# Optimization experiments

Measured on AMD Instinct MI355X. Metric: run time of the kernel, lower is better.

The kernel has to match this reference:

```python
import jax, jax.numpy as jnp
import numpy as np

V, H, S, B, T = 32000, 1024, 512, 16, 128
SOS = 1  # config['special_tokens']['SOS'] assumed = 1


def setup_inputs() -> dict:
    key = jax.random.key(0)
    ks = jax.random.split(key, 16)
    s = 0.02
    return {
        "encoder_outputs": jax.random.normal(ks[0], (B, S, H), jnp.float32),
        "encoder_h": jax.random.normal(ks[1], (1, B, H), jnp.float32),
        "encoder_c": jax.random.normal(ks[2], (1, B, H), jnp.float32),
        "embedding": jax.random.normal(ks[3], (V, H), jnp.float32) * s,
        "Wq": jax.random.normal(ks[4], (H, H), jnp.float32) * s,
        "bq": jnp.zeros((H,), jnp.float32),
        "Wk": jax.random.normal(ks[5], (H, H), jnp.float32) * s,
        "bk": jnp.zeros((H,), jnp.float32),
        "Wv": jax.random.normal(ks[6], (H, H), jnp.float32) * s,
        "bv": jnp.zeros((H,), jnp.float32),
        "W_ih": jax.random.normal(ks[7], (4 * H, 2 * H), jnp.float32) * s,
        "b_ih": jnp.zeros((4 * H,), jnp.float32),
        "W_hh": jax.random.normal(ks[8], (4 * H, H), jnp.float32) * s,
        "b_hh": jnp.zeros((4 * H,), jnp.float32),
        "W_out": jax.random.normal(ks[9], (V, H), jnp.float32) * s,
        "b_out": jnp.zeros((V,), jnp.float32),
    }


def reference(encoder_outputs, encoder_h, encoder_c, embedding,
              Wq, bq, Wk, bk, Wv, bv,
              W_ih, b_ih, W_hh, b_hh, W_out, b_out):
    h0 = encoder_h[0]  # [B,H]
    c0 = encoder_c[0]
    # key/value projections of encoder outputs are constant across steps
    K = jnp.einsum('bsh,dh->bsd', encoder_outputs, Wk) + bk   # [B,S,H]
    Vl = jnp.einsum('bsh,dh->bsd', encoder_outputs, Wv) + bv  # [B,S,H]
    # decoder input is always SOS (source never updates it when target_tensor is None)
    emb = jnp.broadcast_to(embedding[SOS], (h0.shape[0], H))  # [B,H]
    scale = 1.0 / jnp.sqrt(jnp.float32(H))
    # 1x1 look-ahead mask (query seq_len == 1) is a no-op -> omitted

    def step(carry, _):
        h, c = carry
        q = h @ Wq.T + bq                                 # [B,H]
        scores = jnp.einsum('bh,bsh->bs', q, K) * scale   # [B,S]
        w = jax.nn.softmax(scores, axis=-1)
        ctx = jnp.einsum('bs,bsh->bh', w, Vl)             # [B,H]
        x = jnp.concatenate([emb, ctx], axis=-1)          # [B,2H] (embedded, attn)
        gates = x @ W_ih.T + b_ih + h @ W_hh.T + b_hh     # [B,4H]
        i, f, g, o = jnp.split(gates, 4, axis=-1)         # torch LSTM gate order i,f,g,o
        c2 = jax.nn.sigmoid(f) * c + jax.nn.sigmoid(i) * jnp.tanh(g)
        h2 = jax.nn.sigmoid(o) * jnp.tanh(c2)
        logits = h2 @ W_out.T + b_out                     # [B,V]
        return (h2, c2), logits

    (hT, cT), outs = jax.lax.scan(step, (h0, c0), None, length=T)  # outs [T,B,V]
    outs = jnp.transpose(outs, (1, 0, 2))                          # [B,T,V]
    log_probs = jax.nn.log_softmax(outs, axis=-1)
    return log_probs, (hT[None], cT[None])
```

## Files before the change

kernel.cpp:

```cpp
#include <hip/hip_runtime.h>
#include <hip/hip_bf16.h>
#include <math.h>

typedef short short8 __attribute__((ext_vector_type(8)));
typedef short short4v __attribute__((ext_vector_type(4)));
typedef float f32x4 __attribute__((ext_vector_type(4)));
typedef unsigned long long u64;

#define DEVI __device__ __forceinline__

DEVI float bf2f(short s){ union{unsigned u; float f;} x; x.u = ((unsigned)(unsigned short)s) << 16; return x.f; }

DEVI void st_u32v(unsigned* p, unsigned v){ __hip_atomic_store(p, v, __ATOMIC_RELAXED, __HIP_MEMORY_SCOPE_SYSTEM); }
DEVI unsigned ld_u32v(const unsigned* p){ return __hip_atomic_load(p, __ATOMIC_RELAXED, __HIP_MEMORY_SCOPE_SYSTEM); }
DEVI u64  ld_u64v(const u64* p){ return __hip_atomic_load(p, __ATOMIC_RELAXED, __HIP_MEMORY_SCOPE_SYSTEM); }
DEVI unsigned bfbits(float f){ __hip_bfloat16 h = __float2bfloat16(f); unsigned short b; __builtin_memcpy(&b,&h,2); return (unsigned)b; }

constexpr size_t o_wout   = 0;
constexpr size_t o_encbf  = 0;
constexpr size_t o_kbf    = 16777216;
constexpr size_t o_wkbf   = 33554432;
constexpr size_t o_wvbf   = 35651584;
constexpr size_t o_wqtbf  = 37748736;
constexpr size_t o_vt     = 41943040;
constexpr size_t o_kq     = 65536000;
constexpr size_t o_vbf    = o_kq    + 16777216;
constexpr size_t o_wih2   = o_vbf   + 16777216;
constexpr size_t o_whh    = o_wih2  + 8388608;
constexpr size_t o_hall   = o_whh   + 8388608;
constexpr size_t o_gconst = o_hall  + 4194304;
constexpr size_t o_sb     = o_gconst+ 16384;
constexpr size_t o_hv     = o_sb    + 32768;
constexpr size_t o_ev     = o_hv    + 65536;
constexpr size_t o_cv     = o_ev    + 32768;

__global__ void k_convert(const float* __restrict__ src, __hip_bfloat16* __restrict__ dst, int n){
  int i = (blockIdx.x*blockDim.x + threadIdx.x)*4;
  int stride = gridDim.x*blockDim.x*4;
  for (; i < n; i += stride){
    float4 v = *(const float4*)(src+i);
    __hip_bfloat16 o[4] = {__float2bfloat16(v.x),__float2bfloat16(v.y),__float2bfloat16(v.z),__float2bfloat16(v.w)};
    *(short4v*)(dst+i) = *(const short4v*)o;
  }
}

__global__ void k_tcvt(const float* __restrict__ src, __hip_bfloat16* __restrict__ dst){
  __shared__ float tile[64][65];
  int i0 = blockIdx.y*64, j0 = blockIdx.x*64;
  int tr = threadIdx.x >> 6, tc = threadIdx.x & 63;
  for (int p=0;p<16;p++){ int r = p*4 + tr; tile[r][tc] = src[(size_t)(i0+r)*1024 + j0+tc]; }
  __syncthreads();
  for (int p=0;p<16;p++){ int r = p*4 + tr; dst[(size_t)(j0+r)*1024 + i0+tc] = __float2bfloat16(tile[tc][r]); }
}

__global__ void k_extract(const float* __restrict__ src, __hip_bfloat16* __restrict__ dst){
  int i = blockIdx.x*blockDim.x + threadIdx.x;
  int stride = gridDim.x*blockDim.x;
  for (; i < 4096*1024; i += stride){
    int r = i >> 10, c = i & 1023;
    dst[i] = __float2bfloat16(src[((size_t)r << 11) + 1024 + c]);
  }
}

__global__ void k_init(const float* __restrict__ eh, unsigned* __restrict__ base){
  int i = blockIdx.x*blockDim.x + threadIdx.x;
  if (i < 16384) base[i] = bfbits(eh[i]);
  else if (i < 40960) base[i] = 0u;
}

__global__ void k_gconst(const float* __restrict__ emb, const float* __restrict__ Wih,
                         const float* __restrict__ bih, const float* __restrict__ bhh,
                         float* __restrict__ gc){
  int w = threadIdx.x >> 6, lane = threadIdx.x & 63;
  int n = blockIdx.x*4 + w;
  const float* er = emb + 1024;
  const float* wr = Wih + (size_t)n*2048;
  float acc = 0.f;
  for (int q=0;q<16;q++){ int k = lane*16+q; acc += er[k]*wr[k]; }
  for (int off=32; off; off>>=1) acc += __shfl_xor(acc, off);
  if (lane==0) gc[n] = acc + bih[n] + bhh[n];
}

__global__ void k_sb(const __hip_bfloat16* __restrict__ Kb, const float* __restrict__ bq,
                     float* __restrict__ sb){
  int w = threadIdx.x >> 6, lane = threadIdx.x & 63;
  int r = blockIdx.x*4 + w;
  const __hip_bfloat16* kr = Kb + (size_t)r*1024;
  float acc = 0.f;
  for (int q=0;q<16;q++){ int k = lane*16+q; acc += __bfloat162float(kr[k])*bq[k]; }
  for (int off=32; off; off>>=1) acc += __shfl_xor(acc, off);
  if (lane==0) sb[r] = acc * 0.03125f;
}

__global__ void k_vtrans(const __hip_bfloat16* __restrict__ V, __hip_bfloat16* __restrict__ VT){
  __shared__ short t[64][65];
  int b = blockIdx.z, s0 = blockIdx.y*64, h0 = blockIdx.x*64;
  int r = threadIdx.x >> 6, c = threadIdx.x & 63;
  const short* vp = (const short*)V + ((size_t)(b*512 + s0))*1024 + h0;
  #pragma unroll
  for (int p=0;p<16;p++) t[p*4+r][c] = vp[(size_t)(p*4+r)*1024 + c];
  __syncthreads();
  short* op = (short*)VT + ((size_t)(b*1024 + h0))*512 + s0;
  #pragma unroll
  for (int p=0;p<16;p++) op[(size_t)(p*4+r)*512 + c] = t[c][p*4+r];
}

template<int EPI>
__global__ __launch_bounds__(256) void k_gemm(const __hip_bfloat16* __restrict__ A,
    const __hip_bfloat16* __restrict__ Bm, const float* __restrict__ bias,
    void* __restrict__ Cp, int M, int N, int K, float scale){
  __shared__ __hip_bfloat16 sA[128*40];
  __shared__ __hip_bfloat16 sB[128*40];
  int tid = threadIdx.x;
  int lane = tid & 63, w = tid >> 6;
  int wr = w >> 1, wc = w & 1;
  int m0 = blockIdx.y*128, n0 = blockIdx.x*128;
  int lrow = lane & 15, lk = lane >> 4;
  f32x4 acc[4][4] = {};
  for (int k0 = 0; k0 < K; k0 += 32){
    __syncthreads();
    #pragma unroll
    for (int l0 = 0; l0 < 1024; l0 += 256){
      int l = l0 + tid;
      int half = l >> 9;
      int ch = l & 511;
      int row = ch >> 2, seg = ch & 3;
      const __hip_bfloat16* src = half ? (Bm + (size_t)(n0+row)*K + k0 + seg*8)
                                       : (A  + (size_t)(m0+row)*K + k0 + seg*8);
      __hip_bfloat16* dst = (half ? sB : sA) + row*40 + seg*8;
      *(short8*)dst = *(const short8*)src;
    }
    __syncthreads();
    short8 af[4], bfq[4];
    #pragma unroll
    for (int mi=0;mi<4;mi++) af[mi]  = *(short8*)(sA + (wr*64+mi*16+lrow)*40 + lk*8);
    #pragma unroll
    for (int ni=0;ni<4;ni++) bfq[ni] = *(short8*)(sB + (wc*64+ni*16+lrow)*40 + lk*8);
    #pragma unroll
    for (int mi=0;mi<4;mi++)
      #pragma unroll
      for (int ni=0;ni<4;ni++)
        acc[mi][ni] = __builtin_amdgcn_mfma_f32_16x16x32_bf16(af[mi], bfq[ni], acc[mi][ni], 0,0,0);
  }
  int crow0 = (lane>>4)*4;
  int ccol = lane & 15;
  #pragma unroll
  for (int mi=0;mi<4;mi++)
    #pragma unroll
    for (int ni=0;ni<4;ni++){
      int gn = n0 + wc*64 + ni*16 + ccol;
      float bv = bias ? bias[gn] : 0.0f;
      #pragma unroll
      for (int j=0;j<4;j++){
        int gm = m0 + wr*64 + mi*16 + crow0 + j;
        float v = acc[mi][ni][j]*scale + bv;
        if (EPI==0){
          ((__hip_bfloat16*)Cp)[(size_t)gm*N + gn] = __float2bfloat16(v);
        } else {
          int tt = gm >> 4, bb = gm & 15;
          ((float*)Cp)[(size_t)(bb*128+tt)*N + gn] = v;
        }
      }
    }
}

__global__ __launch_bounds__(256, 1) void k_decode(
    const __hip_bfloat16* __restrict__ KQ, const __hip_bfloat16* __restrict__ VT,
    const float* __restrict__ sb, const __hip_bfloat16* __restrict__ Whh,
    const __hip_bfloat16* __restrict__ Wih2, const float* __restrict__ gconst,
    const float* __restrict__ ec,
    unsigned* __restrict__ hv, unsigned* __restrict__ ev,
    unsigned* __restrict__ cv, __hip_bfloat16* __restrict__ hall,
    float* __restrict__ outH, float* __restrict__ outC)
{
  __shared__ __attribute__((aligned(16))) __hip_bfloat16 h4L[4][1032];
  __shared__ __attribute__((aligned(16))) float eL[528];
  __shared__ __attribute__((aligned(16))) float sPf[1024];
  __shared__ float sE[32];
  __shared__ __attribute__((aligned(16))) __hip_bfloat16 sCtx[64];
  __shared__ float sSb[32];
  __shared__ float sGc[64];
  __shared__ float sRed[4];

  const int tid = threadIdx.x;
  const int lane = tid & 63, wv = tid >> 6;
  const int l16 = lane & 15, lhi = lane >> 4;
  const int blk = blockIdx.x;
  const int xcd = blk & 7, slot = blk >> 3;
  const int grp = xcd >> 1, half = xcd & 1;
  const int bloc = half*2 + (slot >> 4);
  const int chunk = slot & 15;
  const int g4 = grp*4;
  const int b = g4 + bloc;
  const int j0 = (half*32 + slot) * 16;

  short8 wfrag[64];
  {
    const __hip_bfloat16* wsrc = (wv < 2) ? Whh : Wih2;
    const int koff = (wv & 1) * 512;
    #pragma unroll
    for (int tt = 0; tt < 4; tt++)
      #pragma unroll
      for (int kt = 0; kt < 16; kt++)
        wfrag[tt*16+kt] = *(const short8*)(wsrc + (size_t)(tt*1024 + j0 + l16)*1024 + koff + kt*32 + lhi*8);
  }
  if (tid < 32) sSb[tid] = sb[b*512 + chunk*32 + tid];
  if (tid < 64) sGc[(tid>>4)*16 + (tid&15)] = gconst[(tid>>4)*1024 + j0 + (tid&15)];
  float creg = 0.f;
  if (tid < 64) creg = ec[(size_t)(g4 + (tid>>4))*1024 + j0 + (tid&15)];

  const __hip_bfloat16* kqBlk = KQ + ((size_t)(b*512 + chunk*32))*1024;
  const int ar = (l16 < 4) ? l16 : 3;
  const short8 zfrag = {};
  f32x4 gacc[4] = {};

  const unsigned* snH = hv + (size_t)g4*1024 + lane*16;
  const unsigned* snE = ev + (size_t)b*512 + (lane & 15)*32;
  const unsigned* snC = cv + (size_t)(g4 + (lane>>4))*1024 + (lane&15)*64;

  for (int st = 0; st < 128; ++st){
    const unsigned wantH = (unsigned)st;
    const unsigned wantN = (unsigned)(st+1);

    { unsigned v; do { v = ld_u32v(snH); } while (!__all((int)((v>>16) == wantH))); }
    {
      const u64* s0 = (const u64*)(hv + (size_t)b*1024) + tid*2;
      u64 a0, a1; bool ok;
      do {
        a0 = ld_u64v(s0); a1 = ld_u64v(s0+1);
        ok = (((unsigned)a0>>16)==wantH) && ((unsigned)(a0>>48)==wantH)
          && (((unsigned)a1>>16)==wantH) && ((unsigned)(a1>>48)==wantH);
      } while(!ok);
      short4v o = { (short)(unsigned)a0, (short)(a0>>32), (short)(unsigned)a1, (short)(a1>>32) };
      *(short4v*)&h4L[bloc][tid*4] = o;
    }
    __syncthreads();
    {
      int row = tid >> 3, kx = tid & 7;
      const __hip_bfloat16* kp = kqBlk + (size_t)row*1024 + kx*8;
      float acc = 0.f;
      #pragma unroll
      for (int q = 0; q < 16; q++){
        short8 kv = *(const short8*)(kp + q*64);
        short8 hv8 = *(const short8*)&h4L[bloc][kx*8 + q*64];
        #pragma unroll
        for (int e2 = 0; e2 < 8; e2++) acc += bf2f(hv8[e2]) * bf2f(kv[e2]);
      }
      acc += __shfl_xor(acc, 1); acc += __shfl_xor(acc, 2); acc += __shfl_xor(acc, 4);
      if (kx == 0)
        st_u32v(&ev[(size_t)b*512 + chunk*32 + row], bfbits(expf(acc + sSb[row])) | (wantN<<16));
    }
    #pragma unroll
    for (int rr = 1; rr < 4; rr++){
      int r = (bloc + rr) & 3;
      const u64* s0 = (const u64*)(hv + (size_t)(g4 + r)*1024) + tid*2;
      u64 a0, a1; bool ok;
      do {
        a0 = ld_u64v(s0); a1 = ld_u64v(s0+1);
        ok = (((unsigned)a0>>16)==wantH) && ((unsigned)(a0>>48)==wantH)
          && (((unsigned)a1>>16)==wantH) && ((unsigned)(a1>>48)==wantH);
      } while(!ok);
      short4v o = { (short)(unsigned)a0, (short)(a0>>32), (short)(unsigned)a1, (short)(a1>>32) };
      *(short4v*)&h4L[r][tid*4] = o;
    }
    __syncthreads();
    if (wv < 2){
      const int ko = (wv & 1) * 512;
      #pragma unroll
      for (int kt = 0; kt < 16; kt++){
        short8 a = *(const short8*)&h4L[ar][ko + kt*32 + lhi*8];
        a = (l16 < 4) ? a : zfrag;
        #pragma unroll
        for (int tt = 0; tt < 4; tt++)
          gacc[tt] = __builtin_amdgcn_mfma_f32_16x16x32_bf16(a, wfrag[tt*16+kt], gacc[tt], 0,0,0);
      }
    }

    { unsigned v; do { v = ld_u32v(snE); } while (!__all((int)((v>>16) == wantN))); }
    {
      const u64* s = (const u64*)(ev + (size_t)b*512) + tid;
      u64 v;
      do { v = ld_u64v(s); }
      while(!((((unsigned)v>>16)==wantN) && ((unsigned)(v>>48)==wantN)));
      float e0 = bf2f((short)(unsigned)v), e1 = bf2f((short)(v>>32));
      int i0 = tid*2, pad = (tid>>6)<<2;
      eL[i0 + pad] = e0; eL[i0+1 + pad] = e1;
      float lp = e0 + e1;
      for (int off=32; off; off>>=1) lp += __shfl_xor(lp, off);
      if (lane == 0) sRed[wv] = lp;
    }
    __syncthreads();
    {
      float Linv = 1.0f/(sRed[0]+sRed[1]+sRed[2]+sRed[3]);
      int hloc = tid >> 2, sc = (tid & 3)*128;
      const __hip_bfloat16* vp = VT + ((size_t)(b*1024 + chunk*64 + hloc))*512 + sc;
      const float* epp = eL + sc + ((sc>>7)<<2);
      float a = 0.f;
      #pragma unroll
      for (int q = 0; q < 16; q++){
        short8 vv = *(const short8*)(vp + q*8);
        float4 e0 = *(const float4*)(epp + q*8);
        float4 e1 = *(const float4*)(epp + q*8 + 4);
        a += e0.x*bf2f(vv[0]) + e0.y*bf2f(vv[1]) + e0.z*bf2f(vv[2]) + e0.w*bf2f(vv[3]);
        a += e1.x*bf2f(vv[4]) + e1.y*bf2f(vv[5]) + e1.z*bf2f(vv[6]) + e1.w*bf2f(vv[7]);
      }
      a += __shfl_xor(a, 1); a += __shfl_xor(a, 2);
      if ((tid & 3) == 0) sCtx[hloc] = __float2bfloat16(a * Linv);
    }
    __syncthreads();
    if (tid < 64){
      unsigned short cbts; __builtin_memcpy(&cbts, &sCtx[tid], 2);
      st_u32v(&cv[(size_t)b*1024 + chunk*64 + tid], (unsigned)cbts | (wantN<<16));
    }

    { unsigned v; do { v = ld_u32v(snC); } while (!__all((int)((v>>16) == wantN))); }
    {
      int r = tid >> 6, c0 = (tid & 63)*16;
      const u64* s = (const u64*)(cv + (size_t)(g4 + r)*1024 + c0);
      u64 v[8]; bool ok;
      do {
        ok = true;
        #pragma unroll
        for (int i=0;i<8;i++) v[i] = ld_u64v(s+i);
        #pragma unroll
        for (int i=0;i<8;i++) ok &= (((unsigned)v[i]>>16)==wantN) && ((unsigned)(v[i]>>48)==wantN);
      } while(!ok);
      #pragma unroll
      for (int i=0;i<8;i++){
        short2 o = { (short)(unsigned)v[i], (short)(v[i]>>32) };
        *(short2*)&h4L[r][c0 + 2*i] = *(short2*)&o;
      }
    }
    __syncthreads();
    if (wv >= 2){
      const int ko = (wv & 1) * 512;
      #pragma unroll
      for (int kt = 0; kt < 16; kt++){
        short8 a = *(const short8*)&h4L[ar][ko + kt*32 + lhi*8];
        a = (l16 < 4) ? a : zfrag;
        #pragma unroll
        for (int tt = 0; tt < 4; tt++)
          gacc[tt] = __builtin_amdgcn_mfma_f32_16x16x32_bf16(a, wfrag[tt*16+kt], gacc[tt], 0,0,0);
      }
    }
    if (lhi == 0){
      #pragma unroll
      for (int tt = 0; tt < 4; tt++)
        *(f32x4*)&sPf[(wv*64 + tt*16 + l16)*4] = gacc[tt];
    }
    #pragma unroll
    for (int tt = 0; tt < 4; tt++) gacc[tt] = (f32x4){0.f,0.f,0.f,0.f};
    __syncthreads();
    if (tid < 64){
      int bb = tid >> 4, jj = tid & 15;
      float gv[4];
      #pragma unroll
      for (int tt = 0; tt < 4; tt++){
        float s = sGc[tt*16 + jj];
        #pragma unroll
        for (int w2 = 0; w2 < 4; w2++) s += sPf[(w2*64 + tt*16 + jj)*4 + bb];
        gv[tt] = s;
      }
      float si = 1.f/(1.f+expf(-gv[0]));
      float sf = 1.f/(1.f+expf(-gv[1]));
      float so = 1.f/(1.f+expf(-gv[3]));
      float c2 = sf*creg + si*tanhf(gv[2]);
      float h2 = so*tanhf(c2);
      creg = c2;
      int gb = g4 + bb;
      unsigned hb = bfbits(h2);
      st_u32v(&hv[(size_t)gb*1024 + j0 + jj], hb | (wantN<<16));
      __hip_bfloat16 hbv; unsigned short hu = (unsigned short)hb; __builtin_memcpy(&hbv, &hu, 2);
      hall[((size_t)(st*16 + gb))*1024 + j0 + jj] = hbv;
      if (st == 127){ outH[gb*1024 + j0 + jj] = h2; outC[gb*1024 + j0 + jj] = c2; }
    }
  }
}

__global__ __launch_bounds__(256) void k_logsm(float* __restrict__ out){
  int row = blockIdx.x;
  float* p = out + (size_t)row*32000;
  int tid = threadIdx.x;
  __shared__ float red[4];
  float s = 0.f;
  for (int i = tid*4; i < 32000; i += 1024){
    float4 v = *(float4*)(p+i);
    s += __expf(v.x)+__expf(v.y)+__expf(v.z)+__expf(v.w);
  }
  for (int off=32; off; off>>=1) s += __shfl_xor(s, off);
  if ((tid&63)==0) red[tid>>6] = s;
  __syncthreads();
  float L = logf(red[0]+red[1]+red[2]+red[3]);
  for (int i = tid*4; i < 32000; i += 1024){
    float4 v = *(float4*)(p+i);
    v.x-=L; v.y-=L; v.z-=L; v.w-=L;
    *(float4*)(p+i) = v;
  }
}

extern "C" void kernel_launch(void* const* d_in, const int* in_sizes, int n_in,
                              void* d_out, int out_size, void* d_ws, size_t ws_size,
                              hipStream_t stream){
  const float* enc = (const float*)d_in[0];
  const float* eh  = (const float*)d_in[1];
  const float* ec  = (const float*)d_in[2];
  const float* emb = (const float*)d_in[3];
  const float* Wq  = (const float*)d_in[4];
  const float* bq  = (const float*)d_in[5];
  const float* Wk  = (const float*)d_in[6];
  const float* bk  = (const float*)d_in[7];
  const float* Wv  = (const float*)d_in[8];
  const float* bv  = (const float*)d_in[9];
  const float* Wih = (const float*)d_in[10];
  const float* bih = (const float*)d_in[11];
  const float* Whh = (const float*)d_in[12];
  const float* bhh = (const float*)d_in[13];
  const float* Wo  = (const float*)d_in[14];
  const float* bo  = (const float*)d_in[15];

  char* ws = (char*)d_ws;
  __hip_bfloat16* encbf = (__hip_bfloat16*)(ws + o_encbf);
  __hip_bfloat16* kbf   = (__hip_bfloat16*)(ws + o_kbf);
  __hip_bfloat16* wkbf  = (__hip_bfloat16*)(ws + o_wkbf);
  __hip_bfloat16* wvbf  = (__hip_bfloat16*)(ws + o_wvbf);
  __hip_bfloat16* wqtbf = (__hip_bfloat16*)(ws + o_wqtbf);
  __hip_bfloat16* vt    = (__hip_bfloat16*)(ws + o_vt);
  __hip_bfloat16* woutbf= (__hip_bfloat16*)(ws + o_wout);
  __hip_bfloat16* kq    = (__hip_bfloat16*)(ws + o_kq);
  __hip_bfloat16* vbf   = (__hip_bfloat16*)(ws + o_vbf);
  __hip_bfloat16* wih2  = (__hip_bfloat16*)(ws + o_wih2);
  __hip_bfloat16* whhbf = (__hip_bfloat16*)(ws + o_whh);
  __hip_bfloat16* hall  = (__hip_bfloat16*)(ws + o_hall);
  float* gconst = (float*)(ws + o_gconst);
  float* sbp    = (float*)(ws + o_sb);
  unsigned* hvp = (unsigned*)(ws + o_hv);
  unsigned* evp = (unsigned*)(ws + o_ev);
  unsigned* cvp = (unsigned*)(ws + o_cv);
  float* outP   = (float*)d_out;
  float* outH   = outP + 65536000;
  float* outC   = outH + 16384;

  k_convert<<<1024,256,0,stream>>>(enc, encbf, 8388608);
  k_convert<<<256,256,0,stream>>>(Wk, wkbf, 1048576);
  k_convert<<<256,256,0,stream>>>(Wv, wvbf, 1048576);
  k_tcvt<<<dim3(16,16),256,0,stream>>>(Wq, wqtbf);
  k_gemm<0><<<dim3(8,64),256,0,stream>>>(encbf, wkbf, bk, kbf, 8192,1024,1024, 1.f);
  k_gemm<0><<<dim3(8,64),256,0,stream>>>(encbf, wvbf, bv, vbf, 8192,1024,1024, 1.f);
  k_gemm<0><<<dim3(8,64),256,0,stream>>>(kbf, wqtbf, (const float*)nullptr, kq, 8192,1024,1024, 0.03125f);
  k_vtrans<<<dim3(16,8,16),256,0,stream>>>(vbf, vt);
  k_sb<<<2048,256,0,stream>>>(kbf, bq, sbp);
  k_extract<<<1024,256,0,stream>>>(Wih, wih2);
  k_convert<<<1024,256,0,stream>>>(Whh, whhbf, 4194304);
  k_gconst<<<1024,256,0,stream>>>(emb, Wih, bih, bhh, gconst);
  k_init<<<160,256,0,stream>>>(eh, hvp);

  {
    const __hip_bfloat16* a_kq = kq; const __hip_bfloat16* a_vt = vt;
    const float* a_sb = sbp; const __hip_bfloat16* a_whh = whhbf;
    const __hip_bfloat16* a_wih = wih2; const float* a_gc = gconst;
    const float* a_ec = ec;
    unsigned* a_h = hvp; unsigned* a_e = evp; unsigned* a_c = cvp;
    __hip_bfloat16* a_ha = hall;
    float* a_oh = outH; float* a_oc = outC;
    void* args[] = { &a_kq, &a_vt, &a_sb, &a_whh, &a_wih, &a_gc, &a_ec,
                     &a_h, &a_e, &a_c, &a_ha, &a_oh, &a_oc };
    hipError_t err = hipLaunchCooperativeKernel((void*)k_decode, dim3(256), dim3(256),
                                                args, 0u, stream);
    if (err != hipSuccess){
      k_decode<<<256,256,0,stream>>>(kq, vt, sbp, whhbf, wih2, gconst, ec,
                                     hvp, evp, cvp, hall, outH, outC);
    }
  }

  k_convert<<<2048,256,0,stream>>>(Wo, woutbf, 32768000);
  k_gemm<1><<<dim3(250,16),256,0,stream>>>(hall, woutbf, bo, d_out, 2048,32000,1024, 1.f);
  k_logsm<<<2048,256,0,stream>>>(outP);
}
```

Measured before the change: 2.635 ms.

## Restructure decode attention into per-chunk partial contexts with unnormalized softmax partials

Attention inside the persistent decode kernel is reorganized. Only 64 of the 256 blocks now compute attention, each over a 128-row chunk of one batch: it computes exp-scores locally and a partial context and partial sum, and publishes them as fp16 values tagged with the step. All blocks then combine the four partials per batch row to form the normalized context. This removes one global exchange per step (exp-scores, then context) and the V transpose kernel. In exchange, attention work is concentrated on fewer blocks, the partials lose precision in fp16, and extra block-wide barriers are added.

```diff
diff --git a/kernel.cpp b/kernel.cpp
--- a/kernel.cpp
+++ b/kernel.cpp
@@ -1,5 +1,6 @@
 #include <hip/hip_runtime.h>
 #include <hip/hip_bf16.h>
+#include <hip/hip_fp16.h>
 #include <math.h>
 
 typedef short short8 __attribute__((ext_vector_type(8)));
@@ -15,6 +16,8 @@
 DEVI unsigned ld_u32v(const unsigned* p){ return __hip_atomic_load(p, __ATOMIC_RELAXED, __HIP_MEMORY_SCOPE_SYSTEM); }
 DEVI u64  ld_u64v(const u64* p){ return __hip_atomic_load(p, __ATOMIC_RELAXED, __HIP_MEMORY_SCOPE_SYSTEM); }
 DEVI unsigned bfbits(float f){ __hip_bfloat16 h = __float2bfloat16(f); unsigned short b; __builtin_memcpy(&b,&h,2); return (unsigned)b; }
+DEVI unsigned f16bits(float f){ __half h = __float2half(f); unsigned short b; __builtin_memcpy(&b,&h,2); return (unsigned)b; }
+DEVI float f16val(unsigned short b){ __half h; __builtin_memcpy(&h,&b,2); return __half2float(h); }
 
 constexpr size_t o_wout   = 0;
 constexpr size_t o_encbf  = 0;
@@ -22,7 +25,6 @@
 constexpr size_t o_wkbf   = 33554432;
 constexpr size_t o_wvbf   = 35651584;
 constexpr size_t o_wqtbf  = 37748736;
-constexpr size_t o_vt     = 41943040;
 constexpr size_t o_kq     = 65536000;
 constexpr size_t o_vbf    = o_kq    + 16777216;
 constexpr size_t o_wih2   = o_vbf   + 16777216;
@@ -31,8 +33,7 @@
 constexpr size_t o_gconst = o_hall  + 4194304;
 constexpr size_t o_sb     = o_gconst+ 16384;
 constexpr size_t o_hv     = o_sb    + 32768;
-constexpr size_t o_ev     = o_hv    + 65536;
-constexpr size_t o_cv     = o_ev    + 32768;
+constexpr size_t o_pv     = o_hv    + 65536;
 
 __global__ void k_convert(const float* __restrict__ src, __hip_bfloat16* __restrict__ dst, int n){
   int i = (blockIdx.x*blockDim.x + threadIdx.x)*4;
@@ -65,7 +66,7 @@
 __global__ void k_init(const float* __restrict__ eh, unsigned* __restrict__ base){
   int i = blockIdx.x*blockDim.x + threadIdx.x;
   if (i < 16384) base[i] = bfbits(eh[i]);
-  else if (i < 40960) base[i] = 0u;
+  else if (i < 82944) base[i] = 0u;
 }
 
 __global__ void k_gconst(const float* __restrict__ emb, const float* __restrict__ Wih,
@@ -90,19 +91,6 @@
   for (int q=0;q<16;q++){ int k = lane*16+q; acc += __bfloat162float(kr[k])*bq[k]; }
   for (int off=32; off; off>>=1) acc += __shfl_xor(acc, off);
   if (lane==0) sb[r] = acc * 0.03125f;
-}
-
-__global__ void k_vtrans(const __hip_bfloat16* __restrict__ V, __hip_bfloat16* __restrict__ VT){
-  __shared__ short t[64][65];
-  int b = blockIdx.z, s0 = blockIdx.y*64, h0 = blockIdx.x*64;
-  int r = threadIdx.x >> 6, c = threadIdx.x & 63;
-  const short* vp = (const short*)V + ((size_t)(b*512 + s0))*1024 + h0;
-  #pragma unroll
-  for (int p=0;p<16;p++) t[p*4+r][c] = vp[(size_t)(p*4+r)*1024 + c];
-  __syncthreads();
-  short* op = (short*)VT + ((size_t)(b*1024 + h0))*512 + s0;
-  #pragma unroll
-  for (int p=0;p<16;p++) op[(size_t)(p*4+r)*512 + c] = t[c][p*4+r];
 }
 
 template<int EPI>
@@ -165,22 +153,20 @@
 }
 
 __global__ __launch_bounds__(256, 1) void k_decode(
-    const __hip_bfloat16* __restrict__ KQ, const __hip_bfloat16* __restrict__ VT,
+    const __hip_bfloat16* __restrict__ KQ, const __hip_bfloat16* __restrict__ Vb,
     const float* __restrict__ sb, const __hip_bfloat16* __restrict__ Whh,
     const __hip_bfloat16* __restrict__ Wih2, const float* __restrict__ gconst,
     const float* __restrict__ ec,
-    unsigned* __restrict__ hv, unsigned* __restrict__ ev,
-    unsigned* __restrict__ cv, __hip_bfloat16* __restrict__ hall,
+    unsigned* __restrict__ hv, unsigned* __restrict__ pv,
+    __hip_bfloat16* __restrict__ hall,
     float* __restrict__ outH, float* __restrict__ outC)
 {
   __shared__ __attribute__((aligned(16))) __hip_bfloat16 h4L[4][1032];
-  __shared__ __attribute__((aligned(16))) float eL[528];
+  __shared__ __attribute__((aligned(16))) float eL[128];
   __shared__ __attribute__((aligned(16))) float sPf[1024];
-  __shared__ float sE[32];
-  __shared__ __attribute__((aligned(16))) __hip_bfloat16 sCtx[64];
-  __shared__ float sSb[32];
+  __shared__ float sSb[128];
   __shared__ float sGc[64];
-  __shared__ float sRed[4];
+  __shared__ float sRed[2];
 
   const int tid = threadIdx.x;
   const int lane = tid & 63, wv = tid >> 6;
@@ -188,11 +174,12 @@
   const int blk = blockIdx.x;
   const int xcd = blk & 7, slot = blk >> 3;
   const int grp = xcd >> 1, half = xcd & 1;
-  const int bloc = half*2 + (slot >> 4);
-  const int chunk = slot & 15;
   const int g4 = grp*4;
-  const int b = g4 + bloc;
   const int j0 = (half*32 + slot) * 16;
+  const bool attA = (slot < 8);
+  const int aid = half*8 + slot;
+  const int bloc = aid >> 2, chunk = aid & 3;
+  const int b_att = g4 + bloc;
 
   short8 wfrag[64];
   {
@@ -204,55 +191,27 @@
       for (int kt = 0; kt < 16; kt++)
         wfrag[tt*16+kt] = *(const short8*)(wsrc + (size_t)(tt*1024 + j0 + l16)*1024 + koff + kt*32 + lhi*8);
   }
-  if (tid < 32) sSb[tid] = sb[b*512 + chunk*32 + tid];
+  if (attA && tid < 128) sSb[tid] = sb[b_att*512 + chunk*128 + tid];
   if (tid < 64) sGc[(tid>>4)*16 + (tid&15)] = gconst[(tid>>4)*1024 + j0 + (tid&15)];
   float creg = 0.f;
   if (tid < 64) creg = ec[(size_t)(g4 + (tid>>4))*1024 + j0 + (tid&15)];
 
-  const __hip_bfloat16* kqBlk = KQ + ((size_t)(b*512 + chunk*32))*1024;
+  const __hip_bfloat16* kqBlk = KQ + ((size_t)(b_att*512 + chunk*128))*1024;
+  const __hip_bfloat16* vBlk  = Vb + ((size_t)(b_att*512 + chunk*128))*1024;
   const int ar = (l16 < 4) ? l16 : 3;
   const short8 zfrag = {};
   f32x4 gacc[4] = {};
 
   const unsigned* snH = hv + (size_t)g4*1024 + lane*16;
-  const unsigned* snE = ev + (size_t)b*512 + (lane & 15)*32;
-  const unsigned* snC = cv + (size_t)(g4 + (lane>>4))*1024 + (lane&15)*64;
+  const unsigned* snP = pv + (size_t)(grp*16 + (lane & 15))*1040;
 
   for (int st = 0; st < 128; ++st){
     const unsigned wantH = (unsigned)st;
     const unsigned wantN = (unsigned)(st+1);
 
     { unsigned v; do { v = ld_u32v(snH); } while (!__all((int)((v>>16) == wantH))); }
-    {
-      const u64* s0 = (const u64*)(hv + (size_t)b*1024) + tid*2;
-      u64 a0, a1; bool ok;
-      do {
-        a0 = ld_u64v(s0); a1 = ld_u64v(s0+1);
-        ok = (((unsigned)a0>>16)==wantH) && ((unsigned)(a0>>48)==wantH)
-          && (((unsigned)a1>>16)==wantH) && ((unsigned)(a1>>48)==wantH);
-      } while(!ok);
-      short4v o = { (short)(unsigned)a0, (short)(a0>>32), (short)(unsigned)a1, (short)(a1>>32) };
-      *(short4v*)&h4L[bloc][tid*4] = o;
-    }
-    __syncthreads();
-    {
-      int row = tid >> 3, kx = tid & 7;
-      const __hip_bfloat16* kp = kqBlk + (size_t)row*1024 + kx*8;
-      float acc = 0.f;
-      #pragma unroll
-      for (int q = 0; q < 16; q++){
-        short8 kv = *(const short8*)(kp + q*64);
-        short8 hv8 = *(const short8*)&h4L[bloc][kx*8 + q*64];
-        #pragma unroll
-        for (int e2 = 0; e2 < 8; e2++) acc += bf2f(hv8[e2]) * bf2f(kv[e2]);
-      }
-      acc += __shfl_xor(acc, 1); acc += __shfl_xor(acc, 2); acc += __shfl_xor(acc, 4);
-      if (kx == 0)
-        st_u32v(&ev[(size_t)b*512 + chunk*32 + row], bfbits(expf(acc + sSb[row])) | (wantN<<16));
-    }
-    #pragma unroll
-    for (int rr = 1; rr < 4; rr++){
-      int r = (bloc + rr) & 3;
+    #pragma unroll
+    for (int r = 0; r < 4; r++){
       const u64* s0 = (const u64*)(hv + (size_t)(g4 + r)*1024) + tid*2;
       u64 a0, a1; bool ok;
       do {
@@ -264,6 +223,49 @@
       *(short4v*)&h4L[r][tid*4] = o;
     }
     __syncthreads();
+
+    if (attA){
+      {
+        int row = tid >> 1, kh = (tid & 1)*512;
+        const __hip_bfloat16* kp = kqBlk + (size_t)row*1024 + kh;
+        const __hip_bfloat16* hp = &h4L[bloc][kh];
+        float acc = 0.f;
+        #pragma unroll
+        for (int q = 0; q < 64; q++){
+          short8 kv = *(const short8*)(kp + q*8);
+          short8 hv8 = *(const short8*)(hp + q*8);
+          #pragma unroll
+          for (int e2 = 0; e2 < 8; e2++) acc += bf2f(hv8[e2]) * bf2f(kv[e2]);
+        }
+        acc += __shfl_xor(acc, 1);
+        if ((tid & 1) == 0) eL[row] = expf(acc + sSb[row]);
+      }
+      __syncthreads();
+      float lp = 0.f;
+      if (tid < 128){
+        lp = eL[tid];
+        for (int off=32; off; off>>=1) lp += __shfl_xor(lp, off);
+        if (lane == 0) sRed[wv] = lp;
+      }
+      __syncthreads();
+      {
+        float Lp = sRed[0] + sRed[1];
+        int d0 = tid*4;
+        float a0=0,a1=0,a2=0,a3=0;
+        const __hip_bfloat16* vp = vBlk + d0;
+        for (int s = 0; s < 128; s++){
+          float ev = eL[s];
+          short4v v4 = *(const short4v*)(vp + (size_t)s*1024);
+          a0 += ev*bf2f(v4[0]); a1 += ev*bf2f(v4[1]); a2 += ev*bf2f(v4[2]); a3 += ev*bf2f(v4[3]);
+        }
+        unsigned* pb = pv + (size_t)(grp*16 + bloc*4 + chunk)*1040;
+        st_u32v(pb + d0,     f16bits(a0) | (wantN<<16));
+        st_u32v(pb + d0 + 1, f16bits(a1) | (wantN<<16));
+        st_u32v(pb + d0 + 2, f16bits(a2) | (wantN<<16));
+        st_u32v(pb + d0 + 3, f16bits(a3) | (wantN<<16));
+        if (tid == 0) st_u32v(pb + 1024, f16bits(Lp) | (wantN<<16));
+      }
+    }
     if (wv < 2){
       const int ko = (wv & 1) * 512;
       #pragma unroll
@@ -275,61 +277,42 @@
           gacc[tt] = __builtin_amdgcn_mfma_f32_16x16x32_bf16(a, wfrag[tt*16+kt], gacc[tt], 0,0,0);
       }
     }
-
-    { unsigned v; do { v = ld_u32v(snE); } while (!__all((int)((v>>16) == wantN))); }
+    __syncthreads();
+
+    { unsigned v; do { v = ld_u32v(snP); } while (!__all((int)((v>>16) == wantN))); }
     {
-      const u64* s = (const u64*)(ev + (size_t)b*512) + tid;
-      u64 v;
-      do { v = ld_u64v(s); }
-      while(!((((unsigned)v>>16)==wantN) && ((unsigned)(v>>48)==wantN)));
-      float e0 = bf2f((short)(unsigned)v), e1 = bf2f((short)(v>>32));
-      int i0 = tid*2, pad = (tid>>6)<<2;
-      eL[i0 + pad] = e0; eL[i0+1 + pad] = e1;
-      float lp = e0 + e1;
-      for (int off=32; off; off>>=1) lp += __shfl_xor(lp, off);
-      if (lane == 0) sRed[wv] = lp;
-    }
-    __syncthreads();
-    {
-      float Linv = 1.0f/(sRed[0]+sRed[1]+sRed[2]+sRed[3]);
-      int hloc = tid >> 2, sc = (tid & 3)*128;
-      const __hip_bfloat16* vp = VT + ((size_t)(b*1024 + chunk*64 + hloc))*512 + sc;
-      const float* epp = eL + sc + ((sc>>7)<<2);
-      float a = 0.f;
-      #pragma unroll
-      for (int q = 0; q < 16; q++){
-        short8 vv = *(const short8*)(vp + q*8);
-        float4 e0 = *(const float4*)(epp + q*8);
-        float4 e1 = *(const float4*)(epp + q*8 + 4);
-        a += e0.x*bf2f(vv[0]) + e0.y*bf2f(vv[1]) + e0.z*bf2f(vv[2]) + e0.w*bf2f(vv[3]);
-        a += e1.x*bf2f(vv[4]) + e1.y*bf2f(vv[5]) + e1.z*bf2f(vv[6]) + e1.w*bf2f(vv[7]);
-      }
-      a += __shfl_xor(a, 1); a += __shfl_xor(a, 2);
-      if ((tid & 3) == 0) sCtx[hloc] = __float2bfloat16(a * Linv);
-    }
-    __syncthreads();
-    if (tid < 64){
-      unsigned short cbts; __builtin_memcpy(&cbts, &sCtx[tid], 2);
-      st_u32v(&cv[(size_t)b*1024 + chunk*64 + tid], (unsigned)cbts | (wantN<<16));
-    }
-
-    { unsigned v; do { v = ld_u32v(snC); } while (!__all((int)((v>>16) == wantN))); }
-    {
-      int r = tid >> 6, c0 = (tid & 63)*16;
-      const u64* s = (const u64*)(cv + (size_t)(g4 + r)*1024 + c0);
-      u64 v[8]; bool ok;
-      do {
-        ok = true;
+      int bi = tid >> 6, dg = tid & 63;
+      float acc[16];
+      #pragma unroll
+      for (int k = 0; k < 16; k++) acc[k] = 0.f;
+      float Lsum = 0.f;
+      #pragma unroll
+      for (int ci = 0; ci < 4; ci++){
+        const unsigned* pb = pv + (size_t)(grp*16 + bi*4 + ci)*1040;
+        const u64* s = (const u64*)(pb + dg*16);
+        u64 v[8]; bool ok;
+        do {
+          ok = true;
+          #pragma unroll
+          for (int i=0;i<8;i++) v[i] = ld_u64v(s+i);
+          #pragma unroll
+          for (int i=0;i<8;i++) ok &= (((unsigned)v[i]>>16)==wantN) && ((unsigned)(v[i]>>48)==wantN);
+        } while(!ok);
         #pragma unroll
-        for (int i=0;i<8;i++) v[i] = ld_u64v(s+i);
-        #pragma unroll
-        for (int i=0;i<8;i++) ok &= (((unsigned)v[i]>>16)==wantN) && ((unsigned)(v[i]>>48)==wantN);
-      } while(!ok);
-      #pragma unroll
-      for (int i=0;i<8;i++){
-        short2 o = { (short)(unsigned)v[i], (short)(v[i]>>32) };
-        *(short2*)&h4L[r][c0 + 2*i] = *(short2*)&o;
-      }
+        for (int i=0;i<8;i++){
+          acc[2*i]   += f16val((unsigned short)(unsigned)v[i]);
+          acc[2*i+1] += f16val((unsigned short)(v[i]>>32));
+        }
+        unsigned lw;
+        do { lw = ld_u32v(pb + 1024); } while ((lw>>16) != wantN);
+        Lsum += f16val((unsigned short)lw);
+      }
+      float Linv = 1.0f / Lsum;
+      __hip_bfloat16 ob[16];
+      #pragma unroll
+      for (int k = 0; k < 16; k++) ob[k] = __float2bfloat16(acc[k]*Linv);
+      *(short8*)&h4L[bi][dg*16]     = *(const short8*)&ob[0];
+      *(short8*)&h4L[bi][dg*16 + 8] = *(const short8*)&ob[8];
     }
     __syncthreads();
     if (wv >= 2){
@@ -374,6 +357,7 @@
       hall[((size_t)(st*16 + gb))*1024 + j0 + jj] = hbv;
       if (st == 127){ outH[gb*1024 + j0 + jj] = h2; outC[gb*1024 + j0 + jj] = c2; }
     }
+    __syncthreads();
   }
 }
 
@@ -424,7 +408,6 @@
   __hip_bfloat16* wkbf  = (__hip_bfloat16*)(ws + o_wkbf);
   __hip_bfloat16* wvbf  = (__hip_bfloat16*)(ws + o_wvbf);
   __hip_bfloat16* wqtbf = (__hip_bfloat16*)(ws + o_wqtbf);
-  __hip_bfloat16* vt    = (__hip_bfloat16*)(ws + o_vt);
   __hip_bfloat16* woutbf= (__hip_bfloat16*)(ws + o_wout);
   __hip_bfloat16* kq    = (__hip_bfloat16*)(ws + o_kq);
   __hip_bfloat16* vbf   = (__hip_bfloat16*)(ws + o_vbf);
@@ -434,8 +417,7 @@
   float* gconst = (float*)(ws + o_gconst);
   float* sbp    = (float*)(ws + o_sb);
   unsigned* hvp = (unsigned*)(ws + o_hv);
-  unsigned* evp = (unsigned*)(ws + o_ev);
-  unsigned* cvp = (unsigned*)(ws + o_cv);
+  unsigned* pvp = (unsigned*)(ws + o_pv);
   float* outP   = (float*)d_out;
   float* outH   = outP + 65536000;
   float* outC   = outH + 16384;
@@ -447,28 +429,27 @@
   k_gemm<0><<<dim3(8,64),256,0,stream>>>(encbf, wkbf, bk, kbf, 8192,1024,1024, 1.f);
   k_gemm<0><<<dim3(8,64),256,0,stream>>>(encbf, wvbf, bv, vbf, 8192,1024,1024, 1.f);
   k_gemm<0><<<dim3(8,64),256,0,stream>>>(kbf, wqtbf, (const float*)nullptr, kq, 8192,1024,1024, 0.03125f);
-  k_vtrans<<<dim3(16,8,16),256,0,stream>>>(vbf, vt);
   k_sb<<<2048,256,0,stream>>>(kbf, bq, sbp);
   k_extract<<<1024,256,0,stream>>>(Wih, wih2);
   k_convert<<<1024,256,0,stream>>>(Whh, whhbf, 4194304);
   k_gconst<<<1024,256,0,stream>>>(emb, Wih, bih, bhh, gconst);
-  k_init<<<160,256,0,stream>>>(eh, hvp);
+  k_init<<<324,256,0,stream>>>(eh, hvp);
 
   {
-    const __hip_bfloat16* a_kq = kq; const __hip_bfloat16* a_vt = vt;
+    const __hip_bfloat16* a_kq = kq; const __hip_bfloat16* a_v = vbf;
     const float* a_sb = sbp; const __hip_bfloat16* a_whh = whhbf;
     const __hip_bfloat16* a_wih = wih2; const float* a_gc = gconst;
     const float* a_ec = ec;
-    unsigned* a_h = hvp; unsigned* a_e = evp; unsigned* a_c = cvp;
+    unsigned* a_h = hvp; unsigned* a_p = pvp;
     __hip_bfloat16* a_ha = hall;
     float* a_oh = outH; float* a_oc = outC;
-    void* args[] = { &a_kq, &a_vt, &a_sb, &a_whh, &a_wih, &a_gc, &a_ec,
-                     &a_h, &a_e, &a_c, &a_ha, &a_oh, &a_oc };
+    void* args[] = { &a_kq, &a_v, &a_sb, &a_whh, &a_wih, &a_gc, &a_ec,
+                     &a_h, &a_p, &a_ha, &a_oh, &a_oc };
     hipError_t err = hipLaunchCooperativeKernel((void*)k_decode, dim3(256), dim3(256),
                                                 args, 0u, stream);
     if (err != hipSuccess){
-      k_decode<<<256,256,0,stream>>>(kq, vt, sbp, whhbf, wih2, gconst, ec,
-                                     hvp, evp, cvp, hall, outH, outC);
+      k_decode<<<256,256,0,stream>>>(kq, vbf, sbp, whhbf, wih2, gconst, ec,
+                                     hvp, pvp, hall, outH, outC);
     }
   }
 
```

Measured after the change: 6.073 ms. +130.5%, slower.

## Fuse log-softmax exp-sums into output GEMM and add local polling in decode

Applied to the files above, without the earlier changes.

The output-projection GEMM epilogue now accumulates per-row partial sums of exp(logits) for each column tile and writes them to a small buffer. A lightweight apply kernel reduces those partials and subtracts the log-sum, so the separate full read of the large logits tensor for the exp reduction goes away. The decode kernel also mirrors attention exp values into a second buffer stored at workgroup scope and polls it with sc0 loads, falling back to system-scope polling after a bounded number of tries. It also drops a shared-memory staging step and barrier for the context vector. The changed polling adds memory-ordering risk and extra stores per step.

```diff
diff --git a/kernel.cpp b/kernel.cpp
--- a/kernel.cpp
+++ b/kernel.cpp
@@ -14,6 +14,13 @@
 DEVI void st_u32v(unsigned* p, unsigned v){ __hip_atomic_store(p, v, __ATOMIC_RELAXED, __HIP_MEMORY_SCOPE_SYSTEM); }
 DEVI unsigned ld_u32v(const unsigned* p){ return __hip_atomic_load(p, __ATOMIC_RELAXED, __HIP_MEMORY_SCOPE_SYSTEM); }
 DEVI u64  ld_u64v(const u64* p){ return __hip_atomic_load(p, __ATOMIC_RELAXED, __HIP_MEMORY_SCOPE_SYSTEM); }
+DEVI void st_u32_wg(unsigned* p, unsigned v){ __hip_atomic_store(p, v, __ATOMIC_RELAXED, __HIP_MEMORY_SCOPE_WORKGROUP); }
+DEVI u64 ld_u64_l2(const u64* p){
+  u64 r;
+  asm volatile("global_load_dwordx2 %0, %1, off sc0\n\ts_waitcnt vmcnt(0)"
+               : "=v"(r) : "v"(p) : "memory");
+  return r;
+}
 DEVI unsigned bfbits(float f){ __hip_bfloat16 h = __float2bfloat16(f); unsigned short b; __builtin_memcpy(&b,&h,2); return (unsigned)b; }
 
 constexpr size_t o_wout   = 0;
@@ -24,6 +31,7 @@
 constexpr size_t o_wqtbf  = 37748736;
 constexpr size_t o_vt     = 41943040;
 constexpr size_t o_kq     = 65536000;
+constexpr size_t o_psum   = o_kq;
 constexpr size_t o_vbf    = o_kq    + 16777216;
 constexpr size_t o_wih2   = o_vbf   + 16777216;
 constexpr size_t o_whh    = o_wih2  + 8388608;
@@ -33,6 +41,7 @@
 constexpr size_t o_hv     = o_sb    + 32768;
 constexpr size_t o_ev     = o_hv    + 65536;
 constexpr size_t o_cv     = o_ev    + 32768;
+constexpr size_t o_evl    = o_cv    + 65536;
 
 __global__ void k_convert(const float* __restrict__ src, __hip_bfloat16* __restrict__ dst, int n){
   int i = (blockIdx.x*blockDim.x + threadIdx.x)*4;
@@ -65,7 +74,7 @@
 __global__ void k_init(const float* __restrict__ eh, unsigned* __restrict__ base){
   int i = blockIdx.x*blockDim.x + threadIdx.x;
   if (i < 16384) base[i] = bfbits(eh[i]);
-  else if (i < 40960) base[i] = 0u;
+  else if (i < 49152) base[i] = 0u;
 }
 
 __global__ void k_gconst(const float* __restrict__ emb, const float* __restrict__ Wih,
@@ -108,9 +117,10 @@
 template<int EPI>
 __global__ __launch_bounds__(256) void k_gemm(const __hip_bfloat16* __restrict__ A,
     const __hip_bfloat16* __restrict__ Bm, const float* __restrict__ bias,
-    void* __restrict__ Cp, int M, int N, int K, float scale){
+    void* __restrict__ Cp, float* __restrict__ psum, int M, int N, int K, float scale){
   __shared__ __hip_bfloat16 sA[128*40];
   __shared__ __hip_bfloat16 sB[128*40];
+  __shared__ float sPart[(EPI==2)?128:1][33];
   int tid = threadIdx.x;
   int lane = tid & 63, w = tid >> 6;
   int wr = w >> 1, wc = w & 1;
@@ -144,6 +154,11 @@
   }
   int crow0 = (lane>>4)*4;
   int ccol = lane & 15;
+  float es[4][4];
+  #pragma unroll
+  for (int mi=0;mi<4;mi++)
+    #pragma unroll
+    for (int j=0;j<4;j++) es[mi][j] = 0.f;
   #pragma unroll
   for (int mi=0;mi<4;mi++)
     #pragma unroll
@@ -159,9 +174,27 @@
         } else {
           int tt = gm >> 4, bb = gm & 15;
           ((float*)Cp)[(size_t)(bb*128+tt)*N + gn] = v;
+          es[mi][j] += __expf(v);
         }
       }
     }
+  if (EPI==2){
+    #pragma unroll
+    for (int mi=0;mi<4;mi++)
+      #pragma unroll
+      for (int j=0;j<4;j++)
+        sPart[wr*64+mi*16+crow0+j][wc*16+ccol] = es[mi][j];
+    __syncthreads();
+    int row = tid >> 1, hh = tid & 1;
+    float s2 = 0.f;
+    #pragma unroll
+    for (int k=0;k<16;k++) s2 += sPart[row][hh*16+k];
+    s2 += __shfl_xor(s2, 1);
+    if (hh == 0){
+      int gm = m0 + row;
+      psum[(size_t)((gm&15)*128 + (gm>>4))*256 + blockIdx.x] = s2;
+    }
+  }
 }
 
 __global__ __launch_bounds__(256, 1) void k_decode(
@@ -170,14 +203,13 @@
     const __hip_bfloat16* __restrict__ Wih2, const float* __restrict__ gconst,
     const float* __restrict__ ec,
     unsigned* __restrict__ hv, unsigned* __restrict__ ev,
-    unsigned* __restrict__ cv, __hip_bfloat16* __restrict__ hall,
+    unsigned* __restrict__ cv, unsigned* __restrict__ evl,
+    __hip_bfloat16* __restrict__ hall,
     float* __restrict__ outH, float* __restrict__ outC)
 {
   __shared__ __attribute__((aligned(16))) __hip_bfloat16 h4L[4][1032];
   __shared__ __attribute__((aligned(16))) float eL[528];
   __shared__ __attribute__((aligned(16))) float sPf[1024];
-  __shared__ float sE[32];
-  __shared__ __attribute__((aligned(16))) __hip_bfloat16 sCtx[64];
   __shared__ float sSb[32];
   __shared__ float sGc[64];
   __shared__ float sRed[4];
@@ -213,6 +245,7 @@
   const int ar = (l16 < 4) ? l16 : 3;
   const short8 zfrag = {};
   f32x4 gacc[4] = {};
+  bool wloc = true;
 
   const unsigned* snH = hv + (size_t)g4*1024 + lane*16;
   const unsigned* snE = ev + (size_t)b*512 + (lane & 15)*32;
@@ -247,8 +280,11 @@
         for (int e2 = 0; e2 < 8; e2++) acc += bf2f(hv8[e2]) * bf2f(kv[e2]);
       }
       acc += __shfl_xor(acc, 1); acc += __shfl_xor(acc, 2); acc += __shfl_xor(acc, 4);
-      if (kx == 0)
-        st_u32v(&ev[(size_t)b*512 + chunk*32 + row], bfbits(expf(acc + sSb[row])) | (wantN<<16));
+      if (kx == 0){
+        unsigned ew = bfbits(expf(acc + sSb[row])) | (wantN<<16);
+        st_u32_wg(&evl[(size_t)b*512 + chunk*32 + row], ew);
+        st_u32v(&ev[(size_t)b*512 + chunk*32 + row], ew);
+      }
     }
     #pragma unroll
     for (int rr = 1; rr < 4; rr++){
@@ -276,12 +312,24 @@
       }
     }
 
-    { unsigned v; do { v = ld_u32v(snE); } while (!__all((int)((v>>16) == wantN))); }
     {
-      const u64* s = (const u64*)(ev + (size_t)b*512) + tid;
-      u64 v;
-      do { v = ld_u64v(s); }
-      while(!((((unsigned)v>>16)==wantN) && ((unsigned)(v>>48)==wantN)));
+      u64 v = 0;
+      if (wloc){
+        const u64* sl = (const u64*)(evl + (size_t)b*512) + tid;
+        int tries = (st == 0) ? 30000 : 4000;
+        bool ok = false;
+        do {
+          v = ld_u64_l2(sl);
+          ok = (((unsigned)v>>16)==wantN) && ((unsigned)(v>>48)==wantN);
+        } while (!__all(ok) && --tries > 0);
+        if (!__all(ok)) wloc = false;
+      }
+      if (!wloc){
+        { unsigned w2; do { w2 = ld_u32v(snE); } while (!__all((int)((w2>>16) == wantN))); }
+        const u64* sg = (const u64*)(ev + (size_t)b*512) + tid;
+        do { v = ld_u64v(sg); }
+        while(!((((unsigned)v>>16)==wantN) && ((unsigned)(v>>48)==wantN)));
+      }
       float e0 = bf2f((short)(unsigned)v), e1 = bf2f((short)(v>>32));
       int i0 = tid*2, pad = (tid>>6)<<2;
       eL[i0 + pad] = e0; eL[i0+1 + pad] = e1;
@@ -305,12 +353,11 @@
         a += e1.x*bf2f(vv[4]) + e1.y*bf2f(vv[5]) + e1.z*bf2f(vv[6]) + e1.w*bf2f(vv[7]);
       }
       a += __shfl_xor(a, 1); a += __shfl_xor(a, 2);
-      if ((tid & 3) == 0) sCtx[hloc] = __float2bfloat16(a * Linv);
-    }
-    __syncthreads();
-    if (tid < 64){
-      unsigned short cbts; __builtin_memcpy(&cbts, &sCtx[tid], 2);
-      st_u32v(&cv[(size_t)b*1024 + chunk*64 + tid], (unsigned)cbts | (wantN<<16));
+      if ((tid & 3) == 0){
+        unsigned short cbts; __hip_bfloat16 cb = __float2bfloat16(a * Linv);
+        __builtin_memcpy(&cbts, &cb, 2);
+        st_u32v(&cv[(size_t)b*1024 + chunk*64 + hloc], (unsigned)cbts | (wantN<<16));
+      }
     }
 
     { unsigned v; do { v = ld_u32v(snC); } while (!__all((int)((v>>16) == wantN))); }
@@ -377,20 +424,16 @@
   }
 }
 
-__global__ __launch_bounds__(256) void k_logsm(float* __restrict__ out){
-  int row = blockIdx.x;
-  float* p = out + (size_t)row*32000;
+__global__ __launch_bounds__(256) void k_apply(float* __restrict__ out, const float* __restrict__ psum){
+  int r = blockIdx.x;
   int tid = threadIdx.x;
   __shared__ float red[4];
-  float s = 0.f;
-  for (int i = tid*4; i < 32000; i += 1024){
-    float4 v = *(float4*)(p+i);
-    s += __expf(v.x)+__expf(v.y)+__expf(v.z)+__expf(v.w);
-  }
+  float s = (tid < 250) ? psum[(size_t)r*256 + tid] : 0.f;
   for (int off=32; off; off>>=1) s += __shfl_xor(s, off);
   if ((tid&63)==0) red[tid>>6] = s;
   __syncthreads();
   float L = logf(red[0]+red[1]+red[2]+red[3]);
+  float* p = out + (size_t)r*32000;
   for (int i = tid*4; i < 32000; i += 1024){
     float4 v = *(float4*)(p+i);
     v.x-=L; v.y-=L; v.z-=L; v.w-=L;
@@ -436,6 +479,8 @@
   unsigned* hvp = (unsigned*)(ws + o_hv);
   unsigned* evp = (unsigned*)(ws + o_ev);
   unsigned* cvp = (unsigned*)(ws + o_cv);
+  unsigned* evlp= (unsigned*)(ws + o_evl);
+  float* psum   = (float*)(ws + o_psum);
   float* outP   = (float*)d_out;
   float* outH   = outP + 65536000;
   float* outC   = outH + 16384;
@@ -444,35 +489,35 @@
   k_convert<<<256,256,0,stream>>>(Wk, wkbf, 1048576);
   k_convert<<<256,256,0,stream>>>(Wv, wvbf, 1048576);
   k_tcvt<<<dim3(16,16),256,0,stream>>>(Wq, wqtbf);
-  k_gemm<0><<<dim3(8,64),256,0,stream>>>(encbf, wkbf, bk, kbf, 8192,1024,1024, 1.f);
-  k_gemm<0><<<dim3(8,64),256,0,stream>>>(encbf, wvbf, bv, vbf, 8192,1024,1024, 1.f);
-  k_gemm<0><<<dim3(8,64),256,0,stream>>>(kbf, wqtbf, (const float*)nullptr, kq, 8192,1024,1024, 0.03125f);
+  k_gemm<0><<<dim3(8,64),256,0,stream>>>(encbf, wkbf, bk, kbf, nullptr, 8192,1024,1024, 1.f);
+  k_gemm<0><<<dim3(8,64),256,0,stream>>>(encbf, wvbf, bv, vbf, nullptr, 8192,1024,1024, 1.f);
+  k_gemm<0><<<dim3(8,64),256,0,stream>>>(kbf, wqtbf, (const float*)nullptr, kq, nullptr, 8192,1024,1024, 0.03125f);
   k_vtrans<<<dim3(16,8,16),256,0,stream>>>(vbf, vt);
   k_sb<<<2048,256,0,stream>>>(kbf, bq, sbp);
   k_extract<<<1024,256,0,stream>>>(Wih, wih2);
   k_convert<<<1024,256,0,stream>>>(Whh, whhbf, 4194304);
   k_gconst<<<1024,256,0,stream>>>(emb, Wih, bih, bhh, gconst);
-  k_init<<<160,256,0,stream>>>(eh, hvp);
+  k_init<<<192,256,0,stream>>>(eh, hvp);
 
   {
     const __hip_bfloat16* a_kq = kq; const __hip_bfloat16* a_vt = vt;
     const float* a_sb = sbp; const __hip_bfloat16* a_whh = whhbf;
     const __hip_bfloat16* a_wih = wih2; const float* a_gc = gconst;
     const float* a_ec = ec;
-    unsigned* a_h = hvp; unsigned* a_e = evp; unsigned* a_c = cvp;
+    unsigned* a_h = hvp; unsigned* a_e = evp; unsigned* a_c = cvp; unsigned* a_el = evlp;
     __hip_bfloat16* a_ha = hall;
     float* a_oh = outH; float* a_oc = outC;
     void* args[] = { &a_kq, &a_vt, &a_sb, &a_whh, &a_wih, &a_gc, &a_ec,
-                     &a_h, &a_e, &a_c, &a_ha, &a_oh, &a_oc };
+                     &a_h, &a_e, &a_c, &a_el, &a_ha, &a_oh, &a_oc };
     hipError_t err = hipLaunchCooperativeKernel((void*)k_decode, dim3(256), dim3(256),
                                                 args, 0u, stream);
     if (err != hipSuccess){
       k_decode<<<256,256,0,stream>>>(kq, vt, sbp, whhbf, wih2, gconst, ec,
-                                     hvp, evp, cvp, hall, outH, outC);
+                                     hvp, evp, cvp, evlp, hall, outH, outC);
     }
   }
 
   k_convert<<<2048,256,0,stream>>>(Wo, woutbf, 32768000);
-  k_gemm<1><<<dim3(250,16),256,0,stream>>>(hall, woutbf, bo, d_out, 2048,32000,1024, 1.f);
-  k_logsm<<<2048,256,0,stream>>>(outP);
-}
+  k_gemm<2><<<dim3(250,16),256,0,stream>>>(hall, woutbf, bo, d_out, psum, 2048,32000,1024, 1.f);
+  k_apply<<<2048,256,0,stream>>>(outP, psum);
+}
```

Result: slower. 5.605 ms (+112.7%).

## Fuse exp-sum partials into output GEMM epilogue to avoid logit re-read

Applied to the files above, without the earlier changes.

The vocab-projection GEMM epilogue now accumulates exp(logit) per row, reduces it across the block through shared memory, and writes one partial sum per row and column tile to a workspace buffer. That buffer reuses the kq region, which is dead after decode. The log-softmax kernel is replaced by k_apply, which sums the 250 partials per row and only subtracts the log-sum-exp. This removes one full read pass over the 262 MB fp32 logits. In exchange it adds exp work and a shared-memory reduction to the GEMM epilogue.

```diff
diff --git a/kernel.cpp b/kernel.cpp
--- a/kernel.cpp
+++ b/kernel.cpp
@@ -24,6 +24,7 @@
 constexpr size_t o_wqtbf  = 37748736;
 constexpr size_t o_vt     = 41943040;
 constexpr size_t o_kq     = 65536000;
+constexpr size_t o_psum   = o_kq;
 constexpr size_t o_vbf    = o_kq    + 16777216;
 constexpr size_t o_wih2   = o_vbf   + 16777216;
 constexpr size_t o_whh    = o_wih2  + 8388608;
@@ -108,9 +109,10 @@
 template<int EPI>
 __global__ __launch_bounds__(256) void k_gemm(const __hip_bfloat16* __restrict__ A,
     const __hip_bfloat16* __restrict__ Bm, const float* __restrict__ bias,
-    void* __restrict__ Cp, int M, int N, int K, float scale){
+    void* __restrict__ Cp, float* __restrict__ psum, int M, int N, int K, float scale){
   __shared__ __hip_bfloat16 sA[128*40];
   __shared__ __hip_bfloat16 sB[128*40];
+  __shared__ float sPart[(EPI==2)?128:1][33];
   int tid = threadIdx.x;
   int lane = tid & 63, w = tid >> 6;
   int wr = w >> 1, wc = w & 1;
@@ -144,6 +146,11 @@
   }
   int crow0 = (lane>>4)*4;
   int ccol = lane & 15;
+  float es[4][4];
+  #pragma unroll
+  for (int mi=0;mi<4;mi++)
+    #pragma unroll
+    for (int j=0;j<4;j++) es[mi][j] = 0.f;
   #pragma unroll
   for (int mi=0;mi<4;mi++)
     #pragma unroll
@@ -159,9 +166,27 @@
         } else {
           int tt = gm >> 4, bb = gm & 15;
           ((float*)Cp)[(size_t)(bb*128+tt)*N + gn] = v;
+          es[mi][j] += __expf(v);
         }
       }
     }
+  if (EPI==2){
+    #pragma unroll
+    for (int mi=0;mi<4;mi++)
+      #pragma unroll
+      for (int j=0;j<4;j++)
+        sPart[wr*64+mi*16+crow0+j][wc*16+ccol] = es[mi][j];
+    __syncthreads();
+    int row = tid >> 1, hh = tid & 1;
+    float s2 = 0.f;
+    #pragma unroll
+    for (int k=0;k<16;k++) s2 += sPart[row][hh*16+k];
+    s2 += __shfl_xor(s2, 1);
+    if (hh == 0){
+      int gm = m0 + row;
+      psum[(size_t)((gm&15)*128 + (gm>>4))*256 + blockIdx.x] = s2;
+    }
+  }
 }
 
 __global__ __launch_bounds__(256, 1) void k_decode(
@@ -176,7 +201,6 @@
   __shared__ __attribute__((aligned(16))) __hip_bfloat16 h4L[4][1032];
   __shared__ __attribute__((aligned(16))) float eL[528];
   __shared__ __attribute__((aligned(16))) float sPf[1024];
-  __shared__ float sE[32];
   __shared__ __attribute__((aligned(16))) __hip_bfloat16 sCtx[64];
   __shared__ float sSb[32];
   __shared__ float sGc[64];
@@ -377,20 +401,16 @@
   }
 }
 
-__global__ __launch_bounds__(256) void k_logsm(float* __restrict__ out){
-  int row = blockIdx.x;
-  float* p = out + (size_t)row*32000;
+__global__ __launch_bounds__(256) void k_apply(float* __restrict__ out, const float* __restrict__ psum){
+  int r = blockIdx.x;
   int tid = threadIdx.x;
   __shared__ float red[4];
-  float s = 0.f;
-  for (int i = tid*4; i < 32000; i += 1024){
-    float4 v = *(float4*)(p+i);
-    s += __expf(v.x)+__expf(v.y)+__expf(v.z)+__expf(v.w);
-  }
+  float s = (tid < 250) ? psum[(size_t)r*256 + tid] : 0.f;
   for (int off=32; off; off>>=1) s += __shfl_xor(s, off);
   if ((tid&63)==0) red[tid>>6] = s;
   __syncthreads();
   float L = logf(red[0]+red[1]+red[2]+red[3]);
+  float* p = out + (size_t)r*32000;
   for (int i = tid*4; i < 32000; i += 1024){
     float4 v = *(float4*)(p+i);
     v.x-=L; v.y-=L; v.z-=L; v.w-=L;
@@ -436,6 +456,7 @@
   unsigned* hvp = (unsigned*)(ws + o_hv);
   unsigned* evp = (unsigned*)(ws + o_ev);
   unsigned* cvp = (unsigned*)(ws + o_cv);
+  float* psum   = (float*)(ws + o_psum);
   float* outP   = (float*)d_out;
   float* outH   = outP + 65536000;
   float* outC   = outH + 16384;
@@ -444,9 +465,9 @@
   k_convert<<<256,256,0,stream>>>(Wk, wkbf, 1048576);
   k_convert<<<256,256,0,stream>>>(Wv, wvbf, 1048576);
   k_tcvt<<<dim3(16,16),256,0,stream>>>(Wq, wqtbf);
-  k_gemm<0><<<dim3(8,64),256,0,stream>>>(encbf, wkbf, bk, kbf, 8192,1024,1024, 1.f);
-  k_gemm<0><<<dim3(8,64),256,0,stream>>>(encbf, wvbf, bv, vbf, 8192,1024,1024, 1.f);
-  k_gemm<0><<<dim3(8,64),256,0,stream>>>(kbf, wqtbf, (const float*)nullptr, kq, 8192,1024,1024, 0.03125f);
+  k_gemm<0><<<dim3(8,64),256,0,stream>>>(encbf, wkbf, bk, kbf, nullptr, 8192,1024,1024, 1.f);
+  k_gemm<0><<<dim3(8,64),256,0,stream>>>(encbf, wvbf, bv, vbf, nullptr, 8192,1024,1024, 1.f);
+  k_gemm<0><<<dim3(8,64),256,0,stream>>>(kbf, wqtbf, (const float*)nullptr, kq, nullptr, 8192,1024,1024, 0.03125f);
   k_vtrans<<<dim3(16,8,16),256,0,stream>>>(vbf, vt);
   k_sb<<<2048,256,0,stream>>>(kbf, bq, sbp);
   k_extract<<<1024,256,0,stream>>>(Wih, wih2);
@@ -473,6 +494,6 @@
   }
 
   k_convert<<<2048,256,0,stream>>>(Wo, woutbf, 32768000);
-  k_gemm<1><<<dim3(250,16),256,0,stream>>>(hall, woutbf, bo, d_out, 2048,32000,1024, 1.f);
-  k_logsm<<<2048,256,0,stream>>>(outP);
-}
+  k_gemm<2><<<dim3(250,16),256,0,stream>>>(hall, woutbf, bo, d_out, psum, 2048,32000,1024, 1.f);
+  k_apply<<<2048,256,0,stream>>>(outP, psum);
+}
```

New measurement: 2.630 ms. Within noise of the previous version (-0.2%).
